# Kernel optimization log

Measured on AMD Instinct MI355X. Metric: run time of the kernel, lower is better.

## Reference

```python
import jax, jax.numpy as jnp
import numpy as np

# CODABlocks (codomain attention) with per_channel_attention=True:
# token_codimension = head_codimension = 1, scale = 2, n_modes = [32, 32],
# mixer_modes = [16, 16], temperature = 1.0, instance_norm (affine) everywhere.
N_HEADS = 16
TEMPERATURE = 1.0
EPS = 1e-5

def _gelu(z):
    return jax.nn.gelu(z, approximate=False)  # matches torch F.gelu default (erf)

def instance_norm(x, g, b):
    # x: (B, C, H, W); normalize over spatial dims per (sample, channel), affine.
    mu = jnp.mean(x, axis=(-2, -1), keepdims=True)
    var = jnp.var(x, axis=(-2, -1), keepdims=True)
    return (x - mu) * jax.lax.rsqrt(var + EPS) * g[:, None, None] + b[:, None, None]

def conv1x1(x, w, b):
    return jnp.einsum('bihw,io->bohw', x, w) + b[None, :, None, None]

def fourier_resample(x, out_shape):
    # FFT-based spatial resampling (mode truncation / zero-pad), norm='forward'.
    if tuple(x.shape[-2:]) == tuple(out_shape):
        return x
    Ho, Wo = out_shape
    xft = jnp.fft.rfftn(x, axes=(-2, -1), norm='forward')
    out = jnp.zeros(x.shape[:-2] + (Ho, Wo // 2 + 1), dtype=xft.dtype)
    hk = min(x.shape[-2], Ho) // 2
    wk = min(xft.shape[-1], Wo // 2 + 1)
    out = out.at[..., :hk, :wk].set(xft[..., :hk, :wk])
    out = out.at[..., -hk:, :wk].set(xft[..., -hk:, :wk])
    return jnp.fft.irfftn(out, s=out_shape, axes=(-2, -1), norm='forward')

def spectral_conv(x, w, out_shape):
    # Truncated-mode spectral convolution (dense weights, equiv. to tucker rank=1.0).
    # w: (Cin, Cout, 2*mh, mw, 2) -> complex weight on kept Fourier modes.
    wc = w[..., 0] + 1j * w[..., 1]
    mh = wc.shape[2] // 2
    mw = wc.shape[3]
    Ho, Wo = out_shape
    xft = jnp.fft.rfftn(x, axes=(-2, -1), norm='forward')   # (B, Cin, H, W//2+1)
    top = jnp.einsum('bihw,iohw->bohw', xft[:, :, :mh, :mw], wc[:, :, :mh])
    bot = jnp.einsum('bihw,iohw->bohw', xft[:, :, -mh:, :mw], wc[:, :, mh:])
    out_ft = jnp.zeros((x.shape[0], wc.shape[1], Ho, Wo // 2 + 1), dtype=xft.dtype)
    out_ft = out_ft.at[:, :, :mh, :mw].set(top)
    out_ft = out_ft.at[:, :, -mh:, :mw].set(bot)
    return jnp.fft.irfftn(out_ft, s=out_shape, axes=(-2, -1), norm='forward')

def fno_layer(x, spec_w, skip_w, skip_b, out_shape, norm=None, act=None):
    # One FNOBlocks layer: spectral conv + (resampled) linear skip, optional norm/act.
    xs = fourier_resample(conv1x1(x, skip_w, skip_b), out_shape)
    xf = spectral_conv(x, spec_w, out_shape)
    if norm is not None:
        xf = instance_norm(xf, *norm)
    y = xf + xs
    return act(y) if act is not None else y

def codano_forward(x, key_w, key_skip_w, key_skip_b, query_w, query_skip_w, query_skip_b, value_w, value_skip_w, value_skip_b, proj_w, proj_skip_w, proj_skip_b, norm1_g, norm1_b, attn_norm_g, attn_norm_b, norm2_g, norm2_b, mixer_w1, mixer_skip_w1, mixer_skip_b1, mixer_norm_g1, mixer_norm_b1, mixer_w2, mixer_skip_w2, mixer_skip_b2, mixer_norm_g2, mixer_norm_b2, mixer_out_g, mixer_out_b):
    b, t, H, W = x.shape   # token codim d = 1 -> channel dim == number of tokens
    tokens = x.reshape(b * t, 1, H, W)
    tokens_norm = instance_norm(tokens, norm1_g, norm1_b)
    Hs, Ws = H // 2, W // 2   # K, Q downsampled by scale = 2
    k = fno_layer(tokens_norm, key_w, key_skip_w, key_skip_b, (Hs, Ws))
    q = fno_layer(tokens_norm, query_w, query_skip_w, query_skip_b, (Hs, Ws))
    v = fno_layer(tokens_norm, value_w, value_skip_w, value_skip_b, (H, W))

    def heads_flat(z):
        hh, ww = z.shape[-2:]
        # (b*t, n_heads*d, h, w) -> (b, heads, t, d*h*w), d = 1
        return z.reshape(b, t, N_HEADS, hh * ww).transpose(0, 2, 1, 3)

    kf, qf, vf = heads_flat(k), heads_flat(q), heads_flat(v)
    scale = jnp.sqrt(jnp.asarray(kf.shape[-1], jnp.float32)) * TEMPERATURE
    dprod = jax.nn.softmax(jnp.einsum('bhtd,bhsd->bhts', qf, kf) / scale, axis=-1)
    attn = jnp.einsum('bhts,bhsd->bhtd', dprod, vf)      # (b, heads, t, H*W)
    attn = attn.transpose(0, 2, 1, 3).reshape(b * t, N_HEADS, H, W)
    # multi-head projection back to token codimension (n_heads -> 1)
    attn = fno_layer(attn, proj_w, proj_skip_w, proj_skip_b, (H, W))
    attn = instance_norm(attn + tokens, attn_norm_g, attn_norm_b)
    # permutation-equivariant mixer: 2 FNO layers shared across all tokens
    m = instance_norm(attn, norm2_g, norm2_b)
    m = fno_layer(m, mixer_w1, mixer_skip_w1, mixer_skip_b1, (H, W), norm=(mixer_norm_g1, mixer_norm_b1), act=_gelu)
    m = fno_layer(m, mixer_w2, mixer_skip_w2, mixer_skip_b2, (H, W), norm=(mixer_norm_g2, mixer_norm_b2))
    out = instance_norm(m, mixer_out_g, mixer_out_b) + attn
    return out.reshape(b, t, H, W)

def setup_inputs():
    key = jax.random.key(0)
    ks = list(jax.random.split(key, 32))
    f32 = jnp.float32
    def W_(k, shape, s=0.02):
        return (s * jax.random.normal(k, shape)).astype(f32)
    B, T, H, Wd = 4, 32, 128, 128
    mh_s, mw_s = 16, 9    # mixer_modes [16,16]: 2*(16//2) rows, 16//2+1 rfft cols
    mh_f, mw_f = 32, 17   # n_modes [32,32]
    return {
        'x': jax.random.normal(ks[0], (B, T, H, Wd), dtype=f32),
        'key_w': W_(ks[1], (1, N_HEADS, mh_s, mw_s, 2)),
        'key_skip_w': W_(ks[2], (1, N_HEADS), 0.5),
        'key_skip_b': W_(ks[3], (N_HEADS,)),
        'query_w': W_(ks[4], (1, N_HEADS, mh_s, mw_s, 2)),
        'query_skip_w': W_(ks[5], (1, N_HEADS), 0.5),
        'query_skip_b': W_(ks[6], (N_HEADS,)),
        'value_w': W_(ks[7], (1, N_HEADS, mh_s, mw_s, 2)),
        'value_skip_w': W_(ks[8], (1, N_HEADS), 0.5),
        'value_skip_b': W_(ks[9], (N_HEADS,)),
        'proj_w': W_(ks[10], (N_HEADS, 1, mh_f, mw_f, 2)),
        'proj_skip_w': W_(ks[11], (N_HEADS, 1), 0.25),
        'proj_skip_b': W_(ks[12], (1,)),
        'norm1_g': jnp.ones((1,), f32), 'norm1_b': jnp.zeros((1,), f32),
        'attn_norm_g': jnp.ones((1,), f32), 'attn_norm_b': jnp.zeros((1,), f32),
        'norm2_g': jnp.ones((1,), f32), 'norm2_b': jnp.zeros((1,), f32),
        'mixer_w1': W_(ks[13], (1, 1, mh_f, mw_f, 2)),
        'mixer_skip_w1': W_(ks[14], (1, 1), 0.5),
        'mixer_skip_b1': W_(ks[15], (1,)),
        'mixer_norm_g1': jnp.ones((1,), f32), 'mixer_norm_b1': jnp.zeros((1,), f32),
        'mixer_w2': W_(ks[16], (1, 1, mh_f, mw_f, 2)),
        'mixer_skip_w2': W_(ks[17], (1, 1), 0.5),
        'mixer_skip_b2': W_(ks[18], (1,)),
        'mixer_norm_g2': jnp.ones((1,), f32), 'mixer_norm_b2': jnp.zeros((1,), f32),
        'mixer_out_g': jnp.ones((1,), f32), 'mixer_out_b': jnp.zeros((1,), f32),
    }

def reference(x, key_w, key_skip_w, key_skip_b, query_w, query_skip_w, query_skip_b, value_w, value_skip_w, value_skip_b, proj_w, proj_skip_w, proj_skip_b, norm1_g, norm1_b, attn_norm_g, attn_norm_b, norm2_g, norm2_b, mixer_w1, mixer_skip_w1, mixer_skip_b1, mixer_norm_g1, mixer_norm_b1, mixer_w2, mixer_skip_w2, mixer_skip_b2, mixer_norm_g2, mixer_norm_b2, mixer_out_g, mixer_out_b):
    return codano_forward(x, key_w, key_skip_w, key_skip_b, query_w, query_skip_w, query_skip_b, value_w, value_skip_w, value_skip_b, proj_w, proj_skip_w, proj_skip_b, norm1_g, norm1_b, attn_norm_g, attn_norm_b, norm2_g, norm2_b, mixer_w1, mixer_skip_w1, mixer_skip_b1, mixer_norm_g1, mixer_norm_b1, mixer_w2, mixer_skip_w2, mixer_skip_b2, mixer_norm_g2, mixer_norm_b2, mixer_out_g, mixer_out_b)
```

## Files before the change

kernel.cpp:

```cpp
#include <hip/hip_runtime.h>
#include <cmath>

#define PI_F 3.14159265358979323846f
#define NTOK 128
#define NPIX 16384
#define NHEADS 16

__device__ __forceinline__ void block_reduce2(float& a, float& b){
  __shared__ float sa[4], sb[4];
  __syncthreads();
  for (int o=32;o>0;o>>=1){ a += __shfl_down(a,o); b += __shfl_down(b,o); }
  int w = threadIdx.x>>6, l = threadIdx.x&63;
  if (l==0){ sa[w]=a; sb[w]=b; }
  __syncthreads();
  a = sa[0]+sa[1]+sa[2]+sa[3];
  b = sb[0]+sb[1]+sb[2]+sb[3];
}

__device__ __forceinline__ float block_reduce1(float a){
  __shared__ float sa[4];
  __syncthreads();
  for (int o=32;o>0;o>>=1) a += __shfl_down(a,o);
  int w = threadIdx.x>>6, l = threadIdx.x&63;
  if (l==0) sa[w]=a;
  __syncthreads();
  return sa[0]+sa[1]+sa[2]+sa[3];
}

__device__ __forceinline__ float gelu_f(float y){
  return 0.5f*y*(1.f + erff(y*0.70710678118f));
}

__device__ __forceinline__ void affine_from(const float* __restrict__ ps, float g, float bb, int t,
                                            float& a, float& b0){
  float sum=0.f,sq=0.f;
  #pragma unroll
  for (int s=0;s<8;s++){ const float* p=ps+((size_t)t*8+s)*2; sum+=p[0]; sq+=p[1]; }
  const float iN=1.f/NPIX;
  float mu=sum*iN, var=sq*iN-mu*mu;
  a=rsqrtf(var+1e-5f)*g;
  b0=bb-mu*a;
}
__device__ __forceinline__ void scalA_from(const float* __restrict__ psA, float ag, float n2g, int t,
                                           float& muZ, float& aA, float& a0){
  float sum=0.f,sq=0.f;
  #pragma unroll
  for (int s=0;s<16;s++){ const float* p=psA+((size_t)t*16+s)*2; sum+=p[0]; sq+=p[1]; }
  const float iN=1.f/NPIX;
  muZ=sum*iN; float var=sq*iN-muZ*muZ;
  float inv=rsqrtf(var+1e-5f);
  aA=inv*ag;
  float var2=aA*aA*var;
  a0=aA*rsqrtf(var2+1e-5f)*n2g;
}
__device__ __forceinline__ void scalB_from(const float* __restrict__ psB, float mng1, int t,
                                           float& mu1, float& c1){
  float sum=0.f,sq=0.f;
  #pragma unroll
  for (int s=0;s<16;s++){ const float* p=psB+((size_t)t*16+s)*2; sum+=p[0]; sq+=p[1]; }
  const float iN=1.f/NPIX;
  mu1=sum*iN; float var=sq*iN-mu1*mu1;
  c1=rsqrtf(var+1e-5f)*mng1;
}
__device__ __forceinline__ void scalC_from(const float* __restrict__ psC, float mng2, float K, float sw,
                                           float outg, int t,
                                           float& mu2f, float& c2, float& mu3, float& c3){
  float sf=0.f,sfsq=0.f,sm=0.f,smsq=0.f,sx=0.f;
  #pragma unroll
  for (int s=0;s<16;s++){
    const float* p=psC+((size_t)t*16+s)*5;
    sf+=p[0]; sfsq+=p[1]; sm+=p[2]; smsq+=p[3]; sx+=p[4];
  }
  const float iN=1.f/NPIX;
  mu2f=sf*iN; float var2=sfsq*iN-mu2f*mu2f;
  c2=rsqrtf(var2+1e-5f)*mng2;
  float Em1=sm*iN, Em1sq=smsq*iN, Exm=sx*iN;
  float Em2=K+sw*Em1;
  float Em2sq = c2*c2*var2 + sw*sw*Em1sq + K*K
              + 2.f*c2*sw*(Exm - mu2f*Em1) + 2.f*K*sw*Em1;
  float var_m2=Em2sq-Em2*Em2;
  mu3=Em2;
  c3=rsqrtf(var_m2+1e-5f)*outg;
}

__global__ __launch_bounds__(256) void k_scol(const float* __restrict__ x,
                        float* __restrict__ A, float* __restrict__ pstat){
  __shared__ float sh[2304];
  int bx=blockIdx.x;
  if (bx<1024){
    float* rows = sh;
    float* tw = sh+2048;
    int base = bx*16;
    for (int i=threadIdx.x;i<2048;i+=256) rows[i] = x[(size_t)base*128 + i];
    for (int p=threadIdx.x;p<128;p+=256){ float sn,cs; sincosf(-(2.f*PI_F/128.f)*(float)p,&sn,&cs); tw[p*2]=cs; tw[p*2+1]=sn; }
    __syncthreads();
    for (int e=threadIdx.x;e<16*33;e+=256){
      int r=e/33, c=e%33;
      const float* rp=rows+r*128;
      float re=0.f, im=0.f;
      for (int w=0;w<128;w++){
        int p=(c*w)&127;
        float v=rp[w];
        re+=v*tw[p*2]; im+=v*tw[p*2+1];
      }
      float* o=A+((size_t)(base+r)*33+c)*2; o[0]=re; o[1]=im;
    }
  } else {
    int u=bx-1024; int t=u>>3, slab=u&7;
    const float* xs = x + (size_t)t*NPIX + slab*2048;
    float sum=0.f, sq=0.f;
    for (int i=threadIdx.x;i<2048;i+=256){ float v=xs[i]; sum+=v; sq+=v*v; }
    block_reduce2(sum,sq);
    if (threadIdx.x==0){ float* o=pstat+((size_t)t*8+slab)*2; o[0]=sum; o[1]=sq; }
  }
}

__global__ __launch_bounds__(256) void k_rowfft64(const float* __restrict__ A,
                          const float* __restrict__ pstat0,
                          const float* __restrict__ n1g, const float* __restrict__ n1b,
                          float* __restrict__ X64, float* __restrict__ X64h){
  int s=blockIdx.x, cg2=blockIdx.y;
  int c0=cg2*11;
  __shared__ float a[128][11][2];
  __shared__ float S[64][11][2];
  __shared__ float tw[128][2];
  for (int i=threadIdx.x;i<128*22;i+=256){
    int r=i/22, q=i%22;
    a[r][q>>1][q&1] = A[((size_t)(s*128+r)*33 + c0)*2 + q];
  }
  for (int p=threadIdx.x;p<128;p+=256){ float sn,cs; sincosf(-(2.f*PI_F/128.f)*(float)p,&sn,&cs); tw[p][0]=cs; tw[p][1]=sn; }
  float af,b0; affine_from(pstat0, n1g[0], n1b[0], s, af, b0);
  __syncthreads();
  const float sc=1.f/16384.f;
  for (int e=threadIdx.x;e<64*11;e+=256){
    int i2=e/11, cl=e%11;
    int r=(i2<32)? i2 : i2+64;
    float re=0.f, im=0.f;
    for (int h=0;h<128;h++){
      int p=(r*h)&127;
      float cs=tw[p][0], sn=tw[p][1];
      float ar=a[h][cl][0], ai=a[h][cl][1];
      re+=ar*cs-ai*sn; im+=ar*sn+ai*cs;
    }
    float vr = af*re*sc, vi = af*im*sc;
    if (r==0 && (c0+cl)==0) vr += b0;
    S[i2][cl][0]=vr; S[i2][cl][1]=vi;
  }
  __syncthreads();
  for (int e=threadIdx.x;e<64*11;e+=256){
    int r=e/11, cl=e%11; int c=c0+cl;
    float vr=S[r][cl][0], vi=S[r][cl][1];
    float* o=X64+((size_t)s*(64*33)+r*33+c)*2; o[0]=vr; o[1]=vi;
    float hr=vr, hi=vi;
    if (c==0 || c==32){
      int pr=(64-r)&63;
      hr=0.5f*(vr+S[pr][cl][0]);
      hi=0.5f*(vi-S[pr][cl][1]);
    }
    float* oh=X64h+((size_t)s*(64*33)+r*33+c)*2; oh[0]=hr; oh[1]=hi;
  }
}

__global__ __launch_bounds__(256) void k_UeZYw(const float* __restrict__ X64, const float* __restrict__ X64h,
    const float* __restrict__ qw, const float* __restrict__ qsw,
    const float* __restrict__ kw, const float* __restrict__ ksw,
    const float* __restrict__ value_w, const float* __restrict__ vsw, const float* __restrict__ vsb,
    const float* __restrict__ proj_w, const float* __restrict__ psw,
    float* __restrict__ Zq, float* __restrict__ Zk, float* __restrict__ Yw,
    float* __restrict__ Ue){
  __shared__ float sh[4224];
  int bx=blockIdx.x;
  if (bx<2048){
    int t=bx>>4, h=bx&15;
    float* Xs = sh;
    float2* xh0 = (float2*)(sh+1092);
    for (int e=threadIdx.x;e<544;e+=256){
      int j=e/17, c=e%17;
      int i2=(j<16)? j : (j+32);
      const float* xp = X64 + ((size_t)t*(64*33) + i2*33 + c)*2;
      Xs[e*2]=xp[0]; Xs[e*2+1]=xp[1];
    }
    if (threadIdx.x<17){
      int j=threadIdx.x;
      int r=(j<=8)? j : j+47;
      const float* hp = X64h + ((size_t)t*(64*33) + r*33)*2;
      xh0[j]=make_float2(hp[0],hp[1]);
    }
    __syncthreads();
    float aq=qsw[h], ak=ksw[h];
    for (int e=threadIdx.x;e<306;e+=256){
      int side=e/153, m=e%153;
      int j=m/9, c=m%9;
      int jj=(j<=8)? j : j+15;
      const float* W = side? kw : qw;
      float a = side? ak : aq;
      float prx=0.f, pry=0.f;
      if (j!=8){
        int jw=(j<8)? j : j-1;
        const float* wp = W + ((size_t)(h*16+jw)*9 + c)*2;
        float xrr=Xs[(jj*17+c)*2], xri=Xs[(jj*17+c)*2+1];
        prx = wp[0]*xrr - wp[1]*xri;
        pry = wp[0]*xri + wp[1]*xrr;
      }
      float Vx=prx, Vy=pry;
      if (c==0){
        int jp = (j==0)? 0 : 17-j;
        float ppx=0.f, ppy=0.f;
        if (jp!=8){
          int jw2=(jp<8)? jp : jp-1;
          const float* wp2 = W + ((size_t)(h*16+jw2)*9)*2;
          int jj2=(jp<=8)? jp : jp+15;
          float x2r=Xs[(jj2*17)*2], x2i=Xs[(jj2*17)*2+1];
          ppx = wp2[0]*x2r - wp2[1]*x2i;
          ppy = wp2[0]*x2i + wp2[1]*x2r;
        }
        Vx = 0.5f*(prx + ppx);
        Vy = 0.5f*(pry - ppy);
      }
      float xmr, xmi;
      if (c==0){ xmr=xh0[j].x; xmi=xh0[j].y; }
      else { xmr=Xs[(jj*17+c)*2]; xmi=Xs[(jj*17+c)*2+1]; }
      float zr = a*xmr + Vx;
      float zi = a*xmi + Vy;
      float wf = (side && c!=0)? 2.f : 1.f;
      float* dst = (side? Zk : Zq) + ((size_t)(t*16+h))*306 + m*2;
      dst[0]=wf*zr; dst[1]=wf*zi;
    }
    int b=t>>5, s=t&31;
    float vw=vsw[h], vb=vsb[h], pw=psw[h];
    size_t obase = ((size_t)(b*16+h)*32 + s)*1088;
    for (int e=threadIdx.x;e<544;e+=256){
      int j=e/17, c=e%17;
      float xr=Xs[e*2], xi=Xs[e*2+1];
      float wvr=0.f,wvi=0.f;
      if (c<=8 && (j<8||j>=24)){
        int jw=(j<8)? j : (j-16);
        const float* wv = value_w + ((size_t)(h*16+jw)*9 + c)*2;
        wvr=wv[0]; wvi=wv[1];
      }
      float Mr=xr*wvr-xi*wvi, Mi=xr*wvi+xi*wvr;
      float Mhr=Mr, Mhi=Mi;
      if (c==0){
        float Pr2=0.f,Pi2=0.f;
        int jp2=(j==0)?0:((j==16)?-1:32-j);
        if (jp2>=0 && (jp2<8||jp2>=24)){
          int jw2=(jp2<8)? jp2 : (jp2-16);
          const float* wv2=value_w+((size_t)(h*16+jw2)*9)*2;
          float pxr=Xs[(jp2*17)*2], pxi=Xs[(jp2*17)*2+1];
          Pr2=pxr*wv2[0]-pxi*wv2[1];
          Pi2=pxr*wv2[1]+pxi*wv2[0];
        }
        Mhr=0.5f*(Mr+Pr2); Mhi=0.5f*(Mi-Pi2);
      }
      float Yr=vw*xr+Mhr+((e==0)? vb:0.f);
      float Yi=vw*xi+Mhi;
      const float* pc=proj_w+((size_t)(h*32+j)*17+c)*2;
      float pr=pc[0], pi=pc[1];
      float* o=Yw+obase+e*2;
      o[0]=pr*Yr-pi*Yi+pw*Mr;
      o[1]=pr*Yi+pi*Yr+pw*Mi;
    }
  } else {
    int u=bx-2048;
    int b=u>>8, rem=u&255, t=rem>>3, sg=rem&7;
    float2* xt=(float2*)sh;
    const float2* src = (const float2*)(X64h + ((size_t)(b*32+t))*4224);
    for (int m=threadIdx.x;m<2112;m+=256){
      int r=m/33, c=m%33;
      bool excl = (c<=8) && (r<=8 || r>=56);
      float w = excl? 0.f : ((c==0||c==32)? 1.f : 2.f);
      float2 v = src[m];
      xt[m]=make_float2(v.x*w, v.y*w);
    }
    __syncthreads();
    float acc[4]={0.f,0.f,0.f,0.f};
    const float2* s0=(const float2*)(X64h + ((size_t)(b*32+sg*4))*4224);
    for (int m=threadIdx.x;m<2112;m+=256){
      float2 a2=xt[m];
      #pragma unroll
      for (int j=0;j<4;j++){
        float2 b2=s0[(size_t)j*2112+m];
        acc[j]+=a2.x*b2.x+a2.y*b2.y;
      }
    }
    for (int j=0;j<4;j++){
      float r=block_reduce1(acc[j]);
      if (threadIdx.x==0) Ue[((size_t)(b*32+t))*32 + sg*4+j]=r;
    }
  }
}

__global__ __launch_bounds__(256) void k_scores2(const float* __restrict__ Zq, const float* __restrict__ Zk,
                          const float* __restrict__ Ue,
                          const float* __restrict__ qsw, const float* __restrict__ qsb,
                          const float* __restrict__ ksw, const float* __restrict__ ksb,
                          float* __restrict__ P){
  int b=blockIdx.x, h=blockIdx.y, tz=blockIdx.z;
  __shared__ float2 zq[16][154];
  __shared__ float2 zk[16][154];
  __shared__ float Pl[16][33];
  for (int i=threadIdx.x;i<16*153;i+=256){
    int t=i/153, m=i%153;
    zq[t][m]=((const float2*)(Zq + ((size_t)((b*32+tz*16+t)*16+h))*306))[m];
  }
  float aq=qsw[h], ak=ksw[h], bq=qsb[h], bk=ksb[h];
  float aqak=aq*ak;
  int tl=threadIdx.x>>4, sl=threadIdx.x&15;
  for (int ch=0; ch<2; ch++){
    __syncthreads();
    for (int i=threadIdx.x;i<16*153;i+=256){
      int s=i/153, m=i%153;
      zk[s][m]=((const float2*)(Zk + ((size_t)((b*32+ch*16+s)*16+h))*306))[m];
    }
    __syncthreads();
    float acc=0.f;
    for (int m=0;m<153;m++){
      float2 a2=zq[tl][m], c2=zk[sl][m];
      acc += a2.x*c2.x + a2.y*c2.y;
    }
    int s=ch*16+sl;
    float G = aqak*Ue[((size_t)(b*32+tz*16+tl))*32+s] + acc;
    Pl[tl][s] = 64.f*(G + bk*zq[tl][0].x + bq*zk[sl][0].x + bq*bk);
  }
  __syncthreads();
  if (threadIdx.x<16){
    int tt=threadIdx.x;
    float mx=-INFINITY;
    for (int s=0;s<32;s++) mx=fmaxf(mx,Pl[tt][s]);
    float e[32]; float sum=0.f;
    for (int s=0;s<32;s++){ e[s]=expf(Pl[tt][s]-mx); sum+=e[s]; }
    float inv=1.f/sum;
    size_t base=((size_t)(b*16+h)*32+tz*16+tt)*32;
    for (int s=0;s<32;s++) P[base+s]=e[s]*inv;
  }
}

__global__ __launch_bounds__(256) void k_SfSk(const float* __restrict__ x, const float* __restrict__ P,
        const float* __restrict__ Yw,
        const float* __restrict__ pw, const float* __restrict__ vw,
        const float* __restrict__ pstat0, const float* __restrict__ n1g, const float* __restrict__ n1b,
        float* __restrict__ Sfp, float* __restrict__ sk){
  __shared__ float sh[4096];
  int bx=blockIdx.x;
  if (bx<272){
    int b=bx/68, rem=bx%68, ec=rem/4, g=rem%4;
    int e0=ec*64, hs0=g*128;
    float (*Pl)[32] = (float(*)[32])sh;
    for (int i=threadIdx.x;i<128*32;i+=256){
      int hsl=i>>5, t=i&31;
      int hs=hs0+hsl, h=hs>>5, s=hs&31;
      Pl[hsl][t]=P[(((size_t)(b*16+h)*32)+t)*32+s];
    }
    __syncthreads();
    int el=threadIdx.x&63, tg=threadIdx.x>>6;
    float acc[8];
    #pragma unroll
    for (int j=0;j<8;j++) acc[j]=0.f;
    const float* Yb = Yw + ((size_t)b*512 + hs0)*1088 + e0 + el;
    #pragma unroll 4
    for (int hsl=0;hsl<128;hsl++){
      float y = Yb[(size_t)hsl*1088];
      #pragma unroll
      for (int j=0;j<8;j++) acc[j] += Pl[hsl][tg*8+j]*y;
    }
    #pragma unroll
    for (int j=0;j<8;j++){
      int t=tg*8+j;
      Sfp[((size_t)(b*32+t)*4+g)*1088 + e0 + el] = acc[j];
    }
  } else {
    int u=bx-272;
    int b=u>>6, rem=u&63, ch=rem>>1, tt=rem&1;
    int pxb=ch*512;
    float* Rs = sh;
    float* cbs = sh+512;
    float* as2 = sh+528;
    float* b0s = sh+560;
    if (threadIdx.x<32){
      float a,b0; affine_from(pstat0, n1g[0], n1b[0], b*32+threadIdx.x, a, b0);
      as2[threadIdx.x]=a; b0s[threadIdx.x]=b0;
    }
    __syncthreads();
    for (int rr=threadIdx.x; rr<512; rr+=256){
      int tl=rr>>5, s=rr&31;
      int t=tt*16+tl;
      float acc=0.f;
      for (int h=0;h<16;h++)
        acc += pw[h]*vw[h]*P[(((size_t)(b*16+h)*32)+t)*32+s];
      Rs[tl*32+s]=acc*as2[s];
      float cb=acc*b0s[s];
      for (int o=16;o>0;o>>=1) cb+=__shfl_down(cb,o,32);
      if (s==0) cbs[tl]=cb;
    }
    __syncthreads();
    float a0[16], a1[16];
    #pragma unroll
    for (int t=0;t<16;t++){ a0[t]=0.f; a1[t]=0.f; }
    for (int s=0;s<32;s++){
      const float* xp = x + ((size_t)(b*32+s))*NPIX + pxb;
      float v0=xp[threadIdx.x], v1=xp[threadIdx.x+256];
      #pragma unroll
      for (int t=0;t<16;t++){ float r=Rs[t*32+s]; a0[t]+=r*v0; a1[t]+=r*v1; }
    }
    #pragma unroll
    for (int t=0;t<16;t++){
      int gt=tt*16+t;
      float cb=cbs[t];
      float* op = sk + ((size_t)(b*32+gt))*NPIX + pxb;
      op[threadIdx.x]=a0[t]+cb; op[threadIdx.x+256]=a1[t]+cb;
    }
  }
}

__global__ __launch_bounds__(256) void k_f0sp(const float* __restrict__ Sfp,
        const float* __restrict__ sk, const float* __restrict__ x,
        const float* __restrict__ P, const float* __restrict__ X64,
        const float* __restrict__ pstat0,
        const float* __restrict__ n1g, const float* __restrict__ n1b,
        const float* __restrict__ pw, const float* __restrict__ vw,
        const float* __restrict__ psw, const float* __restrict__ vsb, const float* __restrict__ psb,
        float* __restrict__ zf, float* __restrict__ pstatA, float* __restrict__ sp){
  __shared__ float sh[1616];
  int bx=blockIdx.x;
  if (bx<2048){
    int bt=bx>>4, slab=bx&15;
    float* Ss=sh; float* T=sh+1088; float* tw=sh+1360;
    for (int i=threadIdx.x;i<1088;i+=256){
      const float* sp4 = Sfp + (size_t)bt*4352 + i;
      Ss[i] = sp4[0]+sp4[1088]+sp4[2176]+sp4[3264];
    }
    for (int p=threadIdx.x;p<128;p+=256){ float sn,cs; sincosf((2.f*PI_F/128.f)*(float)p,&sn,&cs); tw[p*2]=cs; tw[p*2+1]=sn; }
    __syncthreads();
    int h0 = slab*8;
    for (int e=threadIdx.x;e<136;e+=256){
      int hl=e/17, c=e%17; int h=h0+hl;
      float re=0.f, im=0.f;
      for (int j=0;j<32;j++){
        int r=(j<16)? j : (j+96);
        int p=(r*h)&127;
        float cs=tw[p*2], sn=tw[p*2+1];
        float ar=Ss[(j*17+c)*2], ai=Ss[(j*17+c)*2+1];
        re += ar*cs - ai*sn;
        im += ar*sn + ai*cs;
      }
      T[e*2]=re; T[e*2+1]=im;
    }
    __syncthreads();
    size_t base = (size_t)bt*NPIX + h0*128;
    float Cb = psb[0];
    for (int hh=0;hh<16;hh++) Cb += psw[hh]*vsb[hh];
    float sum=0.f, sq=0.f;
    for (int pos=threadIdx.x;pos<1024;pos+=256){
      int hl=pos>>7, w=pos&127;
      const float* Th=T+hl*17*2;
      float br=tw[w*2], bi=tw[w*2+1];
      float rr=br, ri=bi;
      float v=Th[0];
      for (int c=1;c<17;c++){
        v += 2.f*(Th[c*2]*rr - Th[c*2+1]*ri);
        float nr=rr*br-ri*bi; ri=rr*bi+ri*br; rr=nr;
      }
      float val = v + sk[base+pos] + x[base+pos] + Cb;
      zf[base+pos]=val; sum+=val; sq+=val*val;
    }
    block_reduce2(sum,sq);
    if (threadIdx.x==0){ float* o=pstatA+((size_t)bt*16+slab)*2; o[0]=sum; o[1]=sq; }
  } else {
    int u=bx-2048;
    int bt=u>>1, ec=u&1; int b=bt>>5, t=bt&31;
    float* Sfl=sh; float* Rs=sh+1088;
    if (threadIdx.x<32){
      int s=threadIdx.x; float acc=0.f;
      for (int h=0;h<16;h++)
        acc += pw[h]*vw[h]*P[(((size_t)(b*16+h)*32)+t)*32+s];
      Rs[s]=acc;
    }
    for (int i=threadIdx.x;i<1088;i+=256){
      const float* sp4 = Sfp + (size_t)bt*4352 + i;
      Sfl[i]=sp4[0]+sp4[1088]+sp4[2176]+sp4[3264];
    }
    __syncthreads();
    float a_t,b0_t; affine_from(pstat0,n1g[0],n1b[0],bt,a_t,b0_t);
    float Cb=psb[0];
    for (int h=0;h<16;h++) Cb+=psw[h]*vsb[h];
    float inva=1.f/a_t;
    int e1=ec*272, e2=e1+272;
    for (int e=e1+threadIdx.x;e<e2;e+=256){
      int j=e/17, c=e%17;
      float sr=Sfl[e*2], si=Sfl[e*2+1];
      if (c==0){
        if (j==0){ si=0.f; }
        else if (j==16){ sr*=0.5f; si*=0.5f; }
        else { int jp=32-j; sr=0.5f*(sr+Sfl[jp*34]); si=0.5f*(si-Sfl[jp*34+1]); }
      }
      int i2=(j<16)? j : (j+32);
      float re=0.f, im=0.f;
      const float* xb = X64 + ((size_t)(b*32)*(64*33) + i2*33 + c)*2;
      for (int s=0;s<32;s++){
        const float* xp = xb + (size_t)s*(64*33)*2;
        float r=Rs[s];
        re += r*xp[0]; im += r*xp[1];
      }
      const float* xt = X64 + ((size_t)bt*(64*33) + i2*33 + c)*2;
      re += inva*xt[0]; im += inva*xt[1];
      float zr=sr+re, zi=si+im;
      if (e==0) zr += Cb - b0_t*inva;
      sp[((size_t)bt*544+e)*2]=zr; sp[((size_t)bt*544+e)*2+1]=zi;
    }
  }
}

__global__ __launch_bounds__(256) void k_field1(const float* __restrict__ sp, const float* __restrict__ wm,
        const float* __restrict__ pstatA,
        const float* __restrict__ ag, const float* __restrict__ n2g, const float* __restrict__ n2b,
        float* __restrict__ fd1, float* __restrict__ pstatB){
  int bt = blockIdx.x, slab = blockIdx.y;
  __shared__ float Ss[1088];
  __shared__ float T[8*17*2];
  __shared__ float tw[128][2];
  float muZ,aA,a0;
  scalA_from(pstatA, ag[0], n2g[0], bt, muZ, aA, a0);
  float d0 = n2b[0] - muZ*a0;
  for (int e=threadIdx.x;e<544;e+=256){
    float xr=a0*sp[((size_t)bt*544+e)*2] + ((e==0)? d0 : 0.f);
    float xi=a0*sp[((size_t)bt*544+e)*2+1];
    float wr=wm[e*2], wi=wm[e*2+1];
    Ss[e*2]=xr*wr-xi*wi; Ss[e*2+1]=xr*wi+xi*wr;
  }
  for (int p=threadIdx.x;p<128;p+=256){ float sn,cs; sincosf((2.f*PI_F/128.f)*(float)p,&sn,&cs); tw[p][0]=cs; tw[p][1]=sn; }
  __syncthreads();
  int h0 = slab*8;
  for (int e=threadIdx.x;e<8*17;e+=256){
    int hl=e/17, c=e%17; int h=h0+hl;
    float re=0.f, im=0.f;
    for (int j=0;j<32;j++){
      int r=(j<16)? j : (j+96);
      int p=(r*h)&127;
      float cs=tw[p][0], sn=tw[p][1];
      float ar=Ss[(j*17+c)*2], ai=Ss[(j*17+c)*2+1];
      re += ar*cs - ai*sn;
      im += ar*sn + ai*cs;
    }
    T[e*2]=re; T[e*2+1]=im;
  }
  __syncthreads();
  size_t base = (size_t)bt*NPIX + h0*128;
  float sum=0.f, sq=0.f;
  for (int pos=threadIdx.x;pos<1024;pos+=256){
    int hl=pos>>7, w=pos&127;
    const float* Th=T+hl*17*2;
    float br=tw[w][0], bi=tw[w][1];
    float rr=br, ri=bi;
    float v=Th[0];
    for (int c=1;c<17;c++){
      v += 2.f*(Th[c*2]*rr - Th[c*2+1]*ri);
      float nr=rr*br-ri*bi; ri=rr*bi+ri*br; rr=nr;
    }
    fd1[base+pos]=v; sum+=v; sq+=v*v;
  }
  block_reduce2(sum,sq);
  if (threadIdx.x==0){ float* o=pstatB+((size_t)bt*16+slab)*2; o[0]=sum; o[1]=sq; }
}

__global__ __launch_bounds__(256) void k_colA1(const float* __restrict__ f1, const float* __restrict__ z,
        const float* __restrict__ pstatA, const float* __restrict__ pstatB,
        const float* __restrict__ ag, const float* __restrict__ n2g, const float* __restrict__ mng1,
        const float* __restrict__ n2b,
        const float* __restrict__ mnb1, const float* __restrict__ msw1, const float* __restrict__ msb1,
        float* __restrict__ A){
  __shared__ float rows[16*128];
  __shared__ float tw[128][2];
  int grow = blockIdx.x*16;
  int t = grow>>7;
  float muZ,aA,a0;
  scalA_from(pstatA, ag[0], n2g[0], t, muZ, aA, a0);
  float b2 = n2b[0];
  float mu1,c1;
  scalB_from(pstatB, mng1[0], t, mu1, c1);
  float nb=mnb1[0], sw=msw1[0], sb=msb1[0];
  for (int i=threadIdx.x;i<2048;i+=256){
    size_t gi=(size_t)grow*128+i;
    float m0v=(z[gi]-muZ)*a0+b2;
    float y=(f1[gi]-mu1)*c1+nb + m0v*sw + sb;
    rows[i]=gelu_f(y);
  }
  for (int p=threadIdx.x;p<128;p+=256){ float sn,cs; sincosf(-(2.f*PI_F/128.f)*(float)p,&sn,&cs); tw[p][0]=cs; tw[p][1]=sn; }
  __syncthreads();
  for (int e=threadIdx.x;e<16*17;e+=256){
    int r=e/17, c=e%17;
    const float* rp=rows+r*128;
    float re=0.f, im=0.f;
    for (int w=0;w<128;w++){
      int p=(c*w)&127;
      float v=rp[w];
      re+=v*tw[p][0]; im+=v*tw[p][1];
    }
    float* o=A+((size_t)(grow+r)*17+c)*2; o[0]=re; o[1]=im;
  }
}

__global__ __launch_bounds__(256) void k_rowfft32(const float* __restrict__ A, float* __restrict__ spec){
  int s=blockIdx.x, cg2=blockIdx.y;
  int c0 = (cg2==0)? 0 : (1+cg2*4);
  int nc = (cg2==0)? 5 : 4;
  __shared__ float a[128*5*2];
  __shared__ float tw[128][2];
  for (int i=threadIdx.x;i<128*nc*2;i+=256){
    int r=i/(2*nc), q=i%(2*nc);
    a[(r*5+(q>>1))*2+(q&1)] = A[((size_t)(s*128+r)*17 + c0)*2 + q];
  }
  for (int p=threadIdx.x;p<128;p+=256){ float sn,cs; sincosf(-(2.f*PI_F/128.f)*(float)p,&sn,&cs); tw[p][0]=cs; tw[p][1]=sn; }
  __syncthreads();
  const float sc=1.f/16384.f;
  for (int e=threadIdx.x;e<32*nc;e+=256){
    int j=e/nc, cl=e%nc;
    int r=(j<16)? j : (j+96);
    float re=0.f,im=0.f;
    for (int h=0;h<128;h++){
      int p=(r*h)&127;
      float cs=tw[p][0], sn=tw[p][1];
      float ar=a[(h*5+cl)*2], ai=a[(h*5+cl)*2+1];
      re += ar*cs - ai*sn;
      im += ar*sn + ai*cs;
    }
    float* o=spec+((size_t)s*544 + j*17 + c0+cl)*2;
    o[0]=re*sc; o[1]=im*sc;
  }
}

__global__ __launch_bounds__(256) void k_field2(const float* __restrict__ sp2, const float* __restrict__ wm,
        const float* __restrict__ f1, const float* __restrict__ z,
        const float* __restrict__ pstatA, const float* __restrict__ pstatB,
        const float* __restrict__ ag, const float* __restrict__ n2g, const float* __restrict__ mng1,
        const float* __restrict__ n2b, const float* __restrict__ mnb1,
        const float* __restrict__ msw1, const float* __restrict__ msb1,
        float* __restrict__ fd2, float* __restrict__ pstatC){
  int bt = blockIdx.x, slab = blockIdx.y;
  __shared__ float Ss[1088];
  __shared__ float T[8*17*2];
  __shared__ float tw[128][2];
  for (int e=threadIdx.x;e<544;e+=256){
    float xr=sp2[((size_t)bt*544+e)*2], xi=sp2[((size_t)bt*544+e)*2+1];
    float wr=wm[e*2], wi=wm[e*2+1];
    Ss[e*2]=xr*wr-xi*wi; Ss[e*2+1]=xr*wi+xi*wr;
  }
  for (int p=threadIdx.x;p<128;p+=256){ float sn,cs; sincosf((2.f*PI_F/128.f)*(float)p,&sn,&cs); tw[p][0]=cs; tw[p][1]=sn; }
  __syncthreads();
  int h0 = slab*8;
  for (int e=threadIdx.x;e<8*17;e+=256){
    int hl=e/17, c=e%17; int h=h0+hl;
    float re=0.f, im=0.f;
    for (int j=0;j<32;j++){
      int r=(j<16)? j : (j+96);
      int p=(r*h)&127;
      float cs=tw[p][0], sn=tw[p][1];
      float ar=Ss[(j*17+c)*2], ai=Ss[(j*17+c)*2+1];
      re += ar*cs - ai*sn;
      im += ar*sn + ai*cs;
    }
    T[e*2]=re; T[e*2+1]=im;
  }
  __syncthreads();
  size_t base = (size_t)bt*NPIX + h0*128;
  float muZ,aA,a0,mu1,c1;
  scalA_from(pstatA, ag[0], n2g[0], bt, muZ, aA, a0);
  scalB_from(pstatB, mng1[0], bt, mu1, c1);
  float b2=n2b[0], nb1=mnb1[0], sw1=msw1[0], sb1=msb1[0];
  float s_f=0.f,s_fsq=0.f,s_m=0.f,s_msq=0.f,s_x=0.f;
  for (int pos=threadIdx.x;pos<1024;pos+=256){
    int hl=pos>>7, w=pos&127;
    const float* Th=T+hl*17*2;
    float br=tw[w][0], bi=tw[w][1];
    float rr=br, ri=bi;
    float v=Th[0];
    for (int c=1;c<17;c++){
      v += 2.f*(Th[c*2]*rr - Th[c*2+1]*ri);
      float nr=rr*br-ri*bi; ri=rr*bi+ri*br; rr=nr;
    }
    size_t gi=base+pos;
    float m0v=(z[gi]-muZ)*a0+b2;
    float y=(f1[gi]-mu1)*c1+nb1 + m0v*sw1 + sb1;
    float m1v=gelu_f(y);
    fd2[gi]=v;
    s_f+=v; s_fsq+=v*v; s_m+=m1v; s_msq+=m1v*m1v; s_x+=v*m1v;
  }
  block_reduce2(s_f,s_fsq);
  block_reduce2(s_m,s_msq);
  s_x = block_reduce1(s_x);
  if (threadIdx.x==0){
    float* o=pstatC+((size_t)bt*16+slab)*5;
    o[0]=s_f; o[1]=s_fsq; o[2]=s_m; o[3]=s_msq; o[4]=s_x;
  }
}

__global__ __launch_bounds__(256) void k_final2(const float* __restrict__ z, const float* __restrict__ f1,
        const float* __restrict__ f2,
        const float* __restrict__ pstatA, const float* __restrict__ pstatB, const float* __restrict__ pstatC,
        const float* __restrict__ ag, const float* __restrict__ n2g, const float* __restrict__ mng1,
        const float* __restrict__ mng2, const float* __restrict__ outg,
        const float* __restrict__ ab, const float* __restrict__ n2b,
        const float* __restrict__ mnb1, const float* __restrict__ msw1, const float* __restrict__ msb1,
        const float* __restrict__ mnb2, const float* __restrict__ msw2, const float* __restrict__ msb2,
        const float* __restrict__ outb, float* __restrict__ out){
  int bt=blockIdx.x, slab=blockIdx.y;
  float muZ,aA,a0,mu1,c1,mu2f,c2,mu3,c3;
  scalA_from(pstatA, ag[0], n2g[0], bt, muZ, aA, a0);
  scalB_from(pstatB, mng1[0], bt, mu1, c1);
  float sw2=msw2[0], K=mnb2[0]+msb2[0];
  scalC_from(pstatC, mng2[0], K, sw2, outg[0], bt, mu2f, c2, mu3, c3);
  float b1=ab[0], b2=n2b[0], nb1=mnb1[0], sw1=msw1[0], sb1=msb1[0];
  float nb2=mnb2[0], sb2=msb2[0], bo=outb[0];
  size_t base=(size_t)bt*NPIX + (size_t)slab*1024;
  for (int i=threadIdx.x;i<1024;i+=256){
    size_t gi=base+i;
    float zv=z[gi];
    float m0v=(zv-muZ)*a0+b2;
    float a2v=(zv-muZ)*aA+b1;
    float y=(f1[gi]-mu1)*c1+nb1 + m0v*sw1 + sb1;
    float m1v=gelu_f(y);
    float m2v=(f2[gi]-mu2f)*c2+nb2 + m1v*sw2 + sb2;
    out[gi]=(m2v-mu3)*c3+bo+a2v;
  }
}

extern "C" void kernel_launch(void* const* d_in, const int* in_sizes, int n_in,
                              void* d_out, int out_size, void* d_ws, size_t ws_size,
                              hipStream_t stream){
  const float* x        = (const float*)d_in[0];
  const float* key_w    = (const float*)d_in[1];
  const float* key_sw   = (const float*)d_in[2];
  const float* key_sb   = (const float*)d_in[3];
  const float* query_w  = (const float*)d_in[4];
  const float* query_sw = (const float*)d_in[5];
  const float* query_sb = (const float*)d_in[6];
  const float* value_w  = (const float*)d_in[7];
  const float* value_sw = (const float*)d_in[8];
  const float* value_sb = (const float*)d_in[9];
  const float* proj_w   = (const float*)d_in[10];
  const float* proj_sw  = (const float*)d_in[11];
  const float* proj_sb  = (const float*)d_in[12];
  const float* norm1_g  = (const float*)d_in[13];
  const float* norm1_b  = (const float*)d_in[14];
  const float* attn_g   = (const float*)d_in[15];
  const float* attn_b   = (const float*)d_in[16];
  const float* norm2_g  = (const float*)d_in[17];
  const float* norm2_b  = (const float*)d_in[18];
  const float* mw1      = (const float*)d_in[19];
  const float* msw1     = (const float*)d_in[20];
  const float* msb1     = (const float*)d_in[21];
  const float* mng1     = (const float*)d_in[22];
  const float* mnb1     = (const float*)d_in[23];
  const float* mw2      = (const float*)d_in[24];
  const float* msw2     = (const float*)d_in[25];
  const float* msb2     = (const float*)d_in[26];
  const float* mng2     = (const float*)d_in[27];
  const float* mnb2     = (const float*)d_in[28];
  const float* outg     = (const float*)d_in[29];
  const float* outb     = (const float*)d_in[30];
  float* out = (float*)d_out;
  float* ws  = (float*)d_ws;

  size_t off=0;
  float* A   = ws + off; off += (size_t)128*128*33*2;
  float* X64 = ws + off; off += (size_t)128*64*33*2;
  float* X64h= ws + off; off += (size_t)128*64*33*2;
  float* Zq  = ws + off; off += (size_t)128*16*306;
  float* Zk  = ws + off; off += (size_t)128*16*306;
  float* Ue  = ws + off; off += (size_t)4*32*32;
  float* P   = ws + off; off += (size_t)4*16*32*32;
  float* Yw  = ws + off; off += (size_t)2048*1088;
  float* Sfp = ws + off; off += (size_t)128*4*1088;
  float* sk  = ws + off; off += (size_t)128*16384;
  float* zf  = ws + off; off += (size_t)128*16384;
  float* fd1 = ws + off; off += (size_t)128*16384;
  float* fd2 = ws + off; off += (size_t)128*16384;
  float* sp  = ws + off; off += (size_t)128*544*2;
  float* sp2 = ws + off; off += (size_t)128*544*2;
  float* pstat0 = ws + off; off += (size_t)128*8*2;
  float* pstatA = ws + off; off += (size_t)128*16*2;
  float* pstatB = ws + off; off += (size_t)128*16*2;
  float* pstatC = ws + off; off += (size_t)128*16*5;

  k_scol<<<2048,256,0,stream>>>(x, A, pstat0);
  k_rowfft64<<<dim3(128,3),256,0,stream>>>(A, pstat0, norm1_g, norm1_b, X64, X64h);
  k_UeZYw<<<3072,256,0,stream>>>(X64, X64h, query_w, query_sw, key_w, key_sw,
      value_w, value_sw, value_sb, proj_w, proj_sw, Zq, Zk, Yw, Ue);
  k_scores2<<<dim3(4,16,2),256,0,stream>>>(Zq, Zk, Ue, query_sw, query_sb, key_sw, key_sb, P);
  k_SfSk<<<528,256,0,stream>>>(x, P, Yw, proj_sw, value_sw, pstat0, norm1_g, norm1_b, Sfp, sk);
  k_f0sp<<<2304,256,0,stream>>>(Sfp, sk, x, P, X64, pstat0, norm1_g, norm1_b,
      proj_sw, value_sw, proj_sw, value_sb, proj_sb, zf, pstatA, sp);
  k_field1<<<dim3(128,16),256,0,stream>>>(sp, mw1, pstatA, attn_g, norm2_g, norm2_b, fd1, pstatB);
  k_colA1<<<1024,256,0,stream>>>(fd1, zf, pstatA, pstatB, attn_g, norm2_g, mng1,
      norm2_b, mnb1, msw1, msb1, A);
  k_rowfft32<<<dim3(128,4),256,0,stream>>>(A, sp2);
  k_field2<<<dim3(128,16),256,0,stream>>>(sp2, mw2, fd1, zf, pstatA, pstatB,
      attn_g, norm2_g, mng1, norm2_b, mnb1, msw1, msb1, fd2, pstatC);
  k_final2<<<dim3(128,16),256,0,stream>>>(zf, fd1, fd2, pstatA, pstatB, pstatC,
      attn_g, norm2_g, mng1, mng2, outg, attn_b, norm2_b,
      mnb1, msw1, msb1, mnb2, msw2, msb2, outb, out);
}
```

Baseline: 301.9 us.

## Fuse mixer second-layer FFT stages and compute stats spectrally via Parseval

Merges the column DFT and row DFT of the second mixer layer into one kernel per sample, holding the intermediate spectrum in shared memory instead of global memory. The variance of the second spectral-conv field and its cross-term with the GELU activation are computed from spectral coefficients using Parseval, which removes the fd2 field buffer and the separate statistics pass. The final kernel then synthesises the field and applies the norm in one pass, cutting four launches to two. The cost is that the fused FFT kernel runs only 128 blocks, which lowers parallelism.

```diff
diff --git a/kernel.cpp b/kernel.cpp
--- a/kernel.cpp
+++ b/kernel.cpp
@@ -61,26 +61,6 @@
   const float iN=1.f/NPIX;
   mu1=sum*iN; float var=sq*iN-mu1*mu1;
   c1=rsqrtf(var+1e-5f)*mng1;
-}
-__device__ __forceinline__ void scalC_from(const float* __restrict__ psC, float mng2, float K, float sw,
-                                           float outg, int t,
-                                           float& mu2f, float& c2, float& mu3, float& c3){
-  float sf=0.f,sfsq=0.f,sm=0.f,smsq=0.f,sx=0.f;
-  #pragma unroll
-  for (int s=0;s<16;s++){
-    const float* p=psC+((size_t)t*16+s)*5;
-    sf+=p[0]; sfsq+=p[1]; sm+=p[2]; smsq+=p[3]; sx+=p[4];
-  }
-  const float iN=1.f/NPIX;
-  mu2f=sf*iN; float var2=sfsq*iN-mu2f*mu2f;
-  c2=rsqrtf(var2+1e-5f)*mng2;
-  float Em1=sm*iN, Em1sq=smsq*iN, Exm=sx*iN;
-  float Em2=K+sw*Em1;
-  float Em2sq = c2*c2*var2 + sw*sw*Em1sq + K*K
-              + 2.f*c2*sw*(Exm - mu2f*Em1) + 2.f*K*sw*Em1;
-  float var_m2=Em2sq-Em2*Em2;
-  mu3=Em2;
-  c3=rsqrtf(var_m2+1e-5f)*outg;
 }
 
 __global__ __launch_bounds__(256) void k_scol(const float* __restrict__ x,
@@ -562,91 +542,129 @@
   if (threadIdx.x==0){ float* o=pstatB+((size_t)bt*16+slab)*2; o[0]=sum; o[1]=sq; }
 }
 
-__global__ __launch_bounds__(256) void k_colA1(const float* __restrict__ f1, const float* __restrict__ z,
+__global__ __launch_bounds__(256) void k_fft2m1(const float* __restrict__ f1, const float* __restrict__ z,
         const float* __restrict__ pstatA, const float* __restrict__ pstatB,
         const float* __restrict__ ag, const float* __restrict__ n2g, const float* __restrict__ mng1,
         const float* __restrict__ n2b,
         const float* __restrict__ mnb1, const float* __restrict__ msw1, const float* __restrict__ msb1,
-        float* __restrict__ A){
-  __shared__ float rows[16*128];
+        float* __restrict__ sp2, float* __restrict__ pstatM){
+  int t = blockIdx.x;
+  __shared__ float rows[2048];
+  __shared__ float Ab[128*17*2];
   __shared__ float tw[128][2];
-  int grow = blockIdx.x*16;
-  int t = grow>>7;
   float muZ,aA,a0;
   scalA_from(pstatA, ag[0], n2g[0], t, muZ, aA, a0);
   float b2 = n2b[0];
   float mu1,c1;
   scalB_from(pstatB, mng1[0], t, mu1, c1);
   float nb=mnb1[0], sw=msw1[0], sb=msb1[0];
-  for (int i=threadIdx.x;i<2048;i+=256){
-    size_t gi=(size_t)grow*128+i;
-    float m0v=(z[gi]-muZ)*a0+b2;
-    float y=(f1[gi]-mu1)*c1+nb + m0v*sw + sb;
-    rows[i]=gelu_f(y);
-  }
   for (int p=threadIdx.x;p<128;p+=256){ float sn,cs; sincosf(-(2.f*PI_F/128.f)*(float)p,&sn,&cs); tw[p][0]=cs; tw[p][1]=sn; }
-  __syncthreads();
-  for (int e=threadIdx.x;e<16*17;e+=256){
-    int r=e/17, c=e%17;
-    const float* rp=rows+r*128;
+  float sm=0.f, smsq=0.f;
+  for (int chk=0; chk<8; chk++){
+    __syncthreads();
+    int r0 = chk*16;
+    for (int i=threadIdx.x;i<2048;i+=256){
+      size_t gi=((size_t)t*128 + r0)*128 + i;
+      float m0v=(z[gi]-muZ)*a0+b2;
+      float y=(f1[gi]-mu1)*c1+nb + m0v*sw + sb;
+      float m1v=gelu_f(y);
+      rows[i]=m1v; sm+=m1v; smsq+=m1v*m1v;
+    }
+    __syncthreads();
+    for (int e=threadIdx.x;e<16*17;e+=256){
+      int r=e/17, c=e%17;
+      const float* rp=rows+r*128;
+      float re=0.f, im=0.f;
+      for (int w=0;w<128;w++){
+        int p=(c*w)&127;
+        float v=rp[w];
+        re+=v*tw[p][0]; im+=v*tw[p][1];
+      }
+      Ab[((r0+r)*17+c)*2]=re; Ab[((r0+r)*17+c)*2+1]=im;
+    }
+  }
+  __syncthreads();
+  const float sc=1.f/16384.f;
+  for (int e=threadIdx.x;e<544;e+=256){
+    int j=e/17, c=e%17;
+    int r=(j<16)? j : (j+96);
     float re=0.f, im=0.f;
-    for (int w=0;w<128;w++){
-      int p=(c*w)&127;
-      float v=rp[w];
-      re+=v*tw[p][0]; im+=v*tw[p][1];
-    }
-    float* o=A+((size_t)(grow+r)*17+c)*2; o[0]=re; o[1]=im;
-  }
-}
-
-__global__ __launch_bounds__(256) void k_rowfft32(const float* __restrict__ A, float* __restrict__ spec){
-  int s=blockIdx.x, cg2=blockIdx.y;
-  int c0 = (cg2==0)? 0 : (1+cg2*4);
-  int nc = (cg2==0)? 5 : 4;
-  __shared__ float a[128*5*2];
-  __shared__ float tw[128][2];
-  for (int i=threadIdx.x;i<128*nc*2;i+=256){
-    int r=i/(2*nc), q=i%(2*nc);
-    a[(r*5+(q>>1))*2+(q&1)] = A[((size_t)(s*128+r)*17 + c0)*2 + q];
-  }
-  for (int p=threadIdx.x;p<128;p+=256){ float sn,cs; sincosf(-(2.f*PI_F/128.f)*(float)p,&sn,&cs); tw[p][0]=cs; tw[p][1]=sn; }
-  __syncthreads();
-  const float sc=1.f/16384.f;
-  for (int e=threadIdx.x;e<32*nc;e+=256){
-    int j=e/nc, cl=e%nc;
-    int r=(j<16)? j : (j+96);
-    float re=0.f,im=0.f;
     for (int h=0;h<128;h++){
       int p=(r*h)&127;
       float cs=tw[p][0], sn=tw[p][1];
-      float ar=a[(h*5+cl)*2], ai=a[(h*5+cl)*2+1];
+      float ar=Ab[(h*17+c)*2], ai=Ab[(h*17+c)*2+1];
       re += ar*cs - ai*sn;
       im += ar*sn + ai*cs;
     }
-    float* o=spec+((size_t)s*544 + j*17 + c0+cl)*2;
-    o[0]=re*sc; o[1]=im*sc;
-  }
-}
-
-__global__ __launch_bounds__(256) void k_field2(const float* __restrict__ sp2, const float* __restrict__ wm,
+    sp2[((size_t)t*544+e)*2]=re*sc; sp2[((size_t)t*544+e)*2+1]=im*sc;
+  }
+  block_reduce2(sm,smsq);
+  if (threadIdx.x==0){ pstatM[t*2]=sm; pstatM[t*2+1]=smsq; }
+}
+
+__global__ __launch_bounds__(256) void k_final3(const float* __restrict__ sp2, const float* __restrict__ wm,
         const float* __restrict__ f1, const float* __restrict__ z,
-        const float* __restrict__ pstatA, const float* __restrict__ pstatB,
+        const float* __restrict__ pstatA, const float* __restrict__ pstatB, const float* __restrict__ pstatM,
         const float* __restrict__ ag, const float* __restrict__ n2g, const float* __restrict__ mng1,
-        const float* __restrict__ n2b, const float* __restrict__ mnb1,
-        const float* __restrict__ msw1, const float* __restrict__ msb1,
-        float* __restrict__ fd2, float* __restrict__ pstatC){
-  int bt = blockIdx.x, slab = blockIdx.y;
+        const float* __restrict__ mng2, const float* __restrict__ outg,
+        const float* __restrict__ ab, const float* __restrict__ n2b,
+        const float* __restrict__ mnb1, const float* __restrict__ msw1, const float* __restrict__ msb1,
+        const float* __restrict__ mnb2, const float* __restrict__ msw2, const float* __restrict__ msb2,
+        const float* __restrict__ outb, float* __restrict__ out){
+  int bt=blockIdx.x, slab=blockIdx.y;
+  __shared__ float Ms[1088];
   __shared__ float Ss[1088];
   __shared__ float T[8*17*2];
   __shared__ float tw[128][2];
   for (int e=threadIdx.x;e<544;e+=256){
-    float xr=sp2[((size_t)bt*544+e)*2], xi=sp2[((size_t)bt*544+e)*2+1];
+    float mr=sp2[((size_t)bt*544+e)*2], mi=sp2[((size_t)bt*544+e)*2+1];
+    Ms[e*2]=mr; Ms[e*2+1]=mi;
     float wr=wm[e*2], wi=wm[e*2+1];
-    Ss[e*2]=xr*wr-xi*wi; Ss[e*2+1]=xr*wi+xi*wr;
+    Ss[e*2]=mr*wr-mi*wi; Ss[e*2+1]=mr*wi+mi*wr;
   }
   for (int p=threadIdx.x;p<128;p+=256){ float sn,cs; sincosf((2.f*PI_F/128.f)*(float)p,&sn,&cs); tw[p][0]=cs; tw[p][1]=sn; }
   __syncthreads();
-  int h0 = slab*8;
+  float af=0.f, ax=0.f;
+  for (int e=threadIdx.x;e<544;e+=256){
+    int c=e%17;
+    if (c!=0){
+      float sr=Ss[e*2], si=Ss[e*2+1];
+      float mr=Ms[e*2], mi=Ms[e*2+1];
+      af += 2.f*(sr*sr+si*si);
+      ax += 2.f*(sr*mr+si*mi);
+    }
+  }
+  block_reduce2(af,ax);
+  float H00 = Ss[0];
+  float Efsq = H00*H00 + af;
+  float Exm  = H00*Ms[0] + ax;
+  for (int j=1;j<16;j++){
+    int jp=32-j;
+    float hr=0.5f*(Ss[j*34]   + Ss[jp*34]);
+    float hi=0.5f*(Ss[j*34+1] - Ss[jp*34+1]);
+    Efsq += 2.f*(hr*hr+hi*hi);
+    Exm  += 2.f*(hr*Ms[j*34] + hi*Ms[j*34+1]);
+  }
+  {
+    float sr=Ss[16*34], si=Ss[16*34+1];
+    Efsq += 0.5f*(sr*sr+si*si);
+    Exm  += sr*Ms[16*34] + si*Ms[16*34+1];
+  }
+  float muZ,aA,a0; scalA_from(pstatA, ag[0], n2g[0], bt, muZ, aA, a0);
+  float mu1,c1; scalB_from(pstatB, mng1[0], bt, mu1, c1);
+  const float iN=1.f/NPIX;
+  float mu2f = H00;
+  float var2 = Efsq - mu2f*mu2f;
+  float c2 = rsqrtf(var2+1e-5f)*mng2[0];
+  float Em1 = pstatM[bt*2]*iN, Em1sq = pstatM[bt*2+1]*iN;
+  float sw2=msw2[0], K=mnb2[0]+msb2[0];
+  float Em2 = K + sw2*Em1;
+  float Em2sq = c2*c2*var2 + sw2*sw2*Em1sq + K*K
+              + 2.f*c2*sw2*(Exm - mu2f*Em1) + 2.f*K*sw2*Em1;
+  float var_m2 = Em2sq - Em2*Em2;
+  float mu3 = Em2;
+  float c3 = rsqrtf(var_m2+1e-5f)*outg[0];
+  int h0=slab*8;
   for (int e=threadIdx.x;e<8*17;e+=256){
     int hl=e/17, c=e%17; int h=h0+hl;
     float re=0.f, im=0.f;
@@ -661,12 +679,9 @@
     T[e*2]=re; T[e*2+1]=im;
   }
   __syncthreads();
-  size_t base = (size_t)bt*NPIX + h0*128;
-  float muZ,aA,a0,mu1,c1;
-  scalA_from(pstatA, ag[0], n2g[0], bt, muZ, aA, a0);
-  scalB_from(pstatB, mng1[0], bt, mu1, c1);
-  float b2=n2b[0], nb1=mnb1[0], sw1=msw1[0], sb1=msb1[0];
-  float s_f=0.f,s_fsq=0.f,s_m=0.f,s_msq=0.f,s_x=0.f;
+  size_t base=(size_t)bt*NPIX + h0*128;
+  float b1=ab[0], b2=n2b[0], nb1=mnb1[0], sw1=msw1[0], sb1=msb1[0];
+  float nb2=mnb2[0], sb2=msb2[0], bo=outb[0];
   for (int pos=threadIdx.x;pos<1024;pos+=256){
     int hl=pos>>7, w=pos&127;
     const float* Th=T+hl*17*2;
@@ -678,47 +693,12 @@
       float nr=rr*br-ri*bi; ri=rr*bi+ri*br; rr=nr;
     }
     size_t gi=base+pos;
-    float m0v=(z[gi]-muZ)*a0+b2;
-    float y=(f1[gi]-mu1)*c1+nb1 + m0v*sw1 + sb1;
-    float m1v=gelu_f(y);
-    fd2[gi]=v;
-    s_f+=v; s_fsq+=v*v; s_m+=m1v; s_msq+=m1v*m1v; s_x+=v*m1v;
-  }
-  block_reduce2(s_f,s_fsq);
-  block_reduce2(s_m,s_msq);
-  s_x = block_reduce1(s_x);
-  if (threadIdx.x==0){
-    float* o=pstatC+((size_t)bt*16+slab)*5;
-    o[0]=s_f; o[1]=s_fsq; o[2]=s_m; o[3]=s_msq; o[4]=s_x;
-  }
-}
-
-__global__ __launch_bounds__(256) void k_final2(const float* __restrict__ z, const float* __restrict__ f1,
-        const float* __restrict__ f2,
-        const float* __restrict__ pstatA, const float* __restrict__ pstatB, const float* __restrict__ pstatC,
-        const float* __restrict__ ag, const float* __restrict__ n2g, const float* __restrict__ mng1,
-        const float* __restrict__ mng2, const float* __restrict__ outg,
-        const float* __restrict__ ab, const float* __restrict__ n2b,
-        const float* __restrict__ mnb1, const float* __restrict__ msw1, const float* __restrict__ msb1,
-        const float* __restrict__ mnb2, const float* __restrict__ msw2, const float* __restrict__ msb2,
-        const float* __restrict__ outb, float* __restrict__ out){
-  int bt=blockIdx.x, slab=blockIdx.y;
-  float muZ,aA,a0,mu1,c1,mu2f,c2,mu3,c3;
-  scalA_from(pstatA, ag[0], n2g[0], bt, muZ, aA, a0);
-  scalB_from(pstatB, mng1[0], bt, mu1, c1);
-  float sw2=msw2[0], K=mnb2[0]+msb2[0];
-  scalC_from(pstatC, mng2[0], K, sw2, outg[0], bt, mu2f, c2, mu3, c3);
-  float b1=ab[0], b2=n2b[0], nb1=mnb1[0], sw1=msw1[0], sb1=msb1[0];
-  float nb2=mnb2[0], sb2=msb2[0], bo=outb[0];
-  size_t base=(size_t)bt*NPIX + (size_t)slab*1024;
-  for (int i=threadIdx.x;i<1024;i+=256){
-    size_t gi=base+i;
     float zv=z[gi];
     float m0v=(zv-muZ)*a0+b2;
     float a2v=(zv-muZ)*aA+b1;
     float y=(f1[gi]-mu1)*c1+nb1 + m0v*sw1 + sb1;
     float m1v=gelu_f(y);
-    float m2v=(f2[gi]-mu2f)*c2+nb2 + m1v*sw2 + sb2;
+    float m2v=(v-mu2f)*c2+nb2 + m1v*sw2 + sb2;
     out[gi]=(m2v-mu3)*c3+bo+a2v;
   }
 }
@@ -773,13 +753,12 @@
   float* sk  = ws + off; off += (size_t)128*16384;
   float* zf  = ws + off; off += (size_t)128*16384;
   float* fd1 = ws + off; off += (size_t)128*16384;
-  float* fd2 = ws + off; off += (size_t)128*16384;
   float* sp  = ws + off; off += (size_t)128*544*2;
   float* sp2 = ws + off; off += (size_t)128*544*2;
   float* pstat0 = ws + off; off += (size_t)128*8*2;
   float* pstatA = ws + off; off += (size_t)128*16*2;
   float* pstatB = ws + off; off += (size_t)128*16*2;
-  float* pstatC = ws + off; off += (size_t)128*16*5;
+  float* pstatM = ws + off; off += (size_t)128*2;
 
   k_scol<<<2048,256,0,stream>>>(x, A, pstat0);
   k_rowfft64<<<dim3(128,3),256,0,stream>>>(A, pstat0, norm1_g, norm1_b, X64, X64h);
@@ -790,12 +769,9 @@
   k_f0sp<<<2304,256,0,stream>>>(Sfp, sk, x, P, X64, pstat0, norm1_g, norm1_b,
       proj_sw, value_sw, proj_sw, value_sb, proj_sb, zf, pstatA, sp);
   k_field1<<<dim3(128,16),256,0,stream>>>(sp, mw1, pstatA, attn_g, norm2_g, norm2_b, fd1, pstatB);
-  k_colA1<<<1024,256,0,stream>>>(fd1, zf, pstatA, pstatB, attn_g, norm2_g, mng1,
-      norm2_b, mnb1, msw1, msb1, A);
-  k_rowfft32<<<dim3(128,4),256,0,stream>>>(A, sp2);
-  k_field2<<<dim3(128,16),256,0,stream>>>(sp2, mw2, fd1, zf, pstatA, pstatB,
-      attn_g, norm2_g, mng1, norm2_b, mnb1, msw1, msb1, fd2, pstatC);
-  k_final2<<<dim3(128,16),256,0,stream>>>(zf, fd1, fd2, pstatA, pstatB, pstatC,
+  k_fft2m1<<<128,256,0,stream>>>(fd1, zf, pstatA, pstatB, attn_g, norm2_g, mng1,
+      norm2_b, mnb1, msw1, msb1, sp2, pstatM);
+  k_final3<<<dim3(128,16),256,0,stream>>>(sp2, mw2, fd1, zf, pstatA, pstatB, pstatM,
       attn_g, norm2_g, mng1, mng2, outg, attn_b, norm2_b,
       mnb1, msw1, msb1, mnb2, msw2, msb2, outb, out);
 }
```

Result: slower. 349.7 us (+15.8%).
